# Performance work log

Hardware: AMD Instinct MI355X
Metric: run time of the kernel (lower is better)

The kernel has to match this reference:

```python
import math
import jax, jax.numpy as jnp
import numpy as np

B, N, D, H = 2, 2048, 1024, 16

def setup_inputs() -> dict:
    key = jax.random.key(0)
    ks = jax.random.split(key, 5)
    x = jax.random.normal(ks[0], (B, N, D), dtype=jnp.float32)
    # causal mask: True = masked (matches masked_fill semantics)
    mask = jnp.broadcast_to(jnp.triu(jnp.ones((N, N), dtype=bool), k=1), (B, N, N))
    sc = 0.02
    Wqkv = jax.random.normal(ks[1], (3 * D, D), dtype=jnp.float32) * sc
    bqkv = jax.random.normal(ks[2], (3 * D,), dtype=jnp.float32) * sc
    Wo = jax.random.normal(ks[3], (D, D), dtype=jnp.float32) * sc
    bo = jax.random.normal(ks[4], (D,), dtype=jnp.float32) * sc
    return {"x": x, "mask": mask, "Wqkv": Wqkv, "bqkv": bqkv, "Wo": Wo, "bo": bo}

def reference(x, mask, Wqkv, bqkv, Wo, bo):
    b, n, d = x.shape
    h = H
    s = d // h
    qkv = x @ Wqkv.T + bqkv                       # [b, n, 3d]
    q, k, v = jnp.split(qkv, 3, axis=2)           # each [b, n, d]
    def heads(z):
        return z.reshape(b, n, h, s).transpose(0, 2, 1, 3)  # [b, h, n, s]
    q, k, v = heads(q), heads(k), heads(v)
    q = q / jnp.asarray(math.sqrt(s), q.dtype)
    a = jnp.einsum('bhqs,bhks->bhqk', q, k)       # [b, h, n, n]
    a = jnp.where(mask[:, None, :, :], -jnp.inf, a)
    a = jax.nn.softmax(a, axis=-1)
    y = jnp.einsum('bhqk,bhks->bhqs', a, v)       # [b, h, n, s]
    y = y.transpose(0, 2, 1, 3).reshape(b, n, d)
    return y @ Wo.T + bo
```

## Files before the change

kernel.cpp:

```cpp
#include <hip/hip_runtime.h>
#include <hip/hip_bf16.h>
#include <stdint.h>

#define BB 2
#define NN 2048
#define DD 1024
#define HH 16
#define SS 64

typedef short short8 __attribute__((ext_vector_type(8)));
typedef float f32x4 __attribute__((ext_vector_type(4)));

__device__ __forceinline__ float bf2f(uint16_t u) {
    return __uint_as_float(((uint32_t)u) << 16);
}
__device__ __forceinline__ uint16_t f2bf(float f) {
    uint32_t u = __float_as_uint(f);
    return (uint16_t)((u + 0x7FFFu + ((u >> 16) & 1u)) >> 16);
}
__device__ __forceinline__ short8 cvt8(float4 a, float4 b) {
    short8 s;
    s[0] = (short)f2bf(a.x); s[1] = (short)f2bf(a.y);
    s[2] = (short)f2bf(a.z); s[3] = (short)f2bf(a.w);
    s[4] = (short)f2bf(b.x); s[5] = (short)f2bf(b.y);
    s[6] = (short)f2bf(b.z); s[7] = (short)f2bf(b.w);
    return s;
}

__device__ __forceinline__ void load_lds16(const uint16_t* g, uint16_t* l) {
    __builtin_amdgcn_global_load_lds(
        (const __attribute__((address_space(1))) void*)g,
        (__attribute__((address_space(3))) void*)l, 16, 0, 0);
}

#define XE  (4096 * 1024)
#define WQE (3072 * 1024)
#define WOE (1024 * 1024)

__global__ __launch_bounds__(256) void cvt_all(
    const float* __restrict__ x, const float* __restrict__ wq,
    const float* __restrict__ wo, uint16_t* __restrict__ dst)
{
    int i = (blockIdx.x * 256 + threadIdx.x) * 8;
    const float* src;
    int off;
    if (i < XE)            { src = x;  off = i; }
    else if (i < XE + WQE) { src = wq; off = i - XE; }
    else                   { src = wo; off = i - XE - WQE; }
    float4 a = *(const float4*)(src + off);
    float4 b = *(const float4*)(src + off + 4);
    *(short8*)(dst + i) = cvt8(a, b);
}

__global__ __launch_bounds__(256) void gemm_qkv(
    const uint16_t* __restrict__ X, const uint16_t* __restrict__ W,
    const float* __restrict__ bias,
    uint16_t* __restrict__ Qb, uint16_t* __restrict__ Kb, uint16_t* __restrict__ Vt)
{
    __shared__ __align__(16) uint16_t smem[18432];
    uint16_t* As0 = smem;
    uint16_t* As1 = smem + 4096;
    uint16_t* Bs0 = smem + 8192;
    uint16_t* Bs1 = smem + 12288;

    const int tid = threadIdx.x;
    const int w = tid >> 6, l = tid & 63;
    const int lq = l & 15, lg = l >> 4;
    const int wm = w >> 1, wn = w & 1;

    const int flat = blockIdx.x + blockIdx.y * 24;
    const int xcd = flat & 7, g = flat >> 3;
    const int n0 = (xcd * 3 + (g % 3)) * 128;
    const int m0 = (g / 3) * 128;

    f32x4 acc[4][4] = {};

    for (int k0 = 0; k0 < 1024; k0 += 64) {
        __syncthreads();
        #pragma unroll
        for (int j = 0; j < 2; ++j) {
            const int c = (j * 4 + w) * 64 + l;
            const size_t ra = (size_t)(m0 + (c >> 2)) * 1024 + k0 + (c & 3) * 8;
            const size_t rb = (size_t)(n0 + (c >> 2)) * 1024 + k0 + (c & 3) * 8;
            load_lds16(X + ra,      As0 + (j * 4 + w) * 512);
            load_lds16(X + ra + 32, As1 + (j * 4 + w) * 512);
            load_lds16(W + rb,      Bs0 + (j * 4 + w) * 512);
            load_lds16(W + rb + 32, Bs1 + (j * 4 + w) * 512);
        }
        __syncthreads();
        short8 af[4], bfr[4];
        #pragma unroll
        for (int mi = 0; mi < 4; ++mi)
            af[mi] = *(const short8*)&As0[(wm * 64 + mi * 16 + lq) * 32 + lg * 8];
        #pragma unroll
        for (int ni = 0; ni < 4; ++ni)
            bfr[ni] = *(const short8*)&Bs0[(wn * 64 + ni * 16 + lq) * 32 + lg * 8];
        #pragma unroll
        for (int mi = 0; mi < 4; ++mi)
            #pragma unroll
            for (int ni = 0; ni < 4; ++ni)
                acc[mi][ni] = __builtin_amdgcn_mfma_f32_16x16x32_bf16(
                    af[mi], bfr[ni], acc[mi][ni], 0, 0, 0);
        #pragma unroll
        for (int mi = 0; mi < 4; ++mi)
            af[mi] = *(const short8*)&As1[(wm * 64 + mi * 16 + lq) * 32 + lg * 8];
        #pragma unroll
        for (int ni = 0; ni < 4; ++ni)
            bfr[ni] = *(const short8*)&Bs1[(wn * 64 + ni * 16 + lq) * 32 + lg * 8];
        #pragma unroll
        for (int mi = 0; mi < 4; ++mi)
            #pragma unroll
            for (int ni = 0; ni < 4; ++ni)
                acc[mi][ni] = __builtin_amdgcn_mfma_f32_16x16x32_bf16(
                    af[mi], bfr[ni], acc[mi][ni], 0, 0, 0);
    }

    __syncthreads();
    const int part = n0 >> 10;
    const int hh = ((n0 + wn * 64) & 1023) >> 6;
    const int mrow0 = m0 + wm * 64;
    const int bh = (mrow0 >> 11) * 16 + hh;
    const int tok0 = mrow0 & 2047;
    const float scl = (part == 0) ? 0.125f * 1.44269504089f : 1.0f;

    float bias4[4];
    #pragma unroll
    for (int ni = 0; ni < 4; ++ni)
        bias4[ni] = bias[n0 + wn * 64 + ni * 16 + lq];

    uint16_t* T = smem + w * 4608;
    if (part < 2) {
        #pragma unroll
        for (int mi = 0; mi < 4; ++mi)
            #pragma unroll
            for (int ni = 0; ni < 4; ++ni)
                #pragma unroll
                for (int r = 0; r < 4; ++r)
                    T[(mi * 16 + lg * 4 + r) * 72 + ni * 16 + lq] =
                        f2bf((acc[mi][ni][r] + bias4[ni]) * scl);
    } else {
        #pragma unroll
        for (int mi = 0; mi < 4; ++mi)
            #pragma unroll
            for (int ni = 0; ni < 4; ++ni)
                #pragma unroll
                for (int r = 0; r < 4; ++r)
                    T[(ni * 16 + lq) * 72 + mi * 16 + lg * 4 + r] =
                        f2bf(acc[mi][ni][r] + bias4[ni]);
    }

    const int a0 = l >> 3, b8 = (l & 7) * 8;
    #pragma unroll
    for (int i = 0; i < 8; ++i) {
        int a = i * 8 + a0;
        short8 u = *(short8*)&T[a * 72 + b8];
        uint16_t* p;
        if (part < 2) {
            uint16_t* dst = (part == 0) ? Qb : Kb;
            p = dst + ((size_t)bh * 2048 + tok0 + a) * 64 + b8;
        } else {
            p = Vt + ((size_t)bh * 64 + a) * 2048 + tok0 + b8;
        }
        *(short8*)p = u;
    }
}

__device__ __forceinline__ void loadK8(const uint16_t* kp, short8 (&d)[8]) {
    #pragma unroll
    for (int n = 0; n < 4; ++n) {
        d[2 * n]     = *(const short8*)(kp + n * 1024);
        d[2 * n + 1] = *(const short8*)(kp + n * 1024 + 32);
    }
}
__device__ __forceinline__ void loadV8(const uint16_t* vp, short8 (&d)[8]) {
    #pragma unroll
    for (int n = 0; n < 4; ++n) {
        d[2 * n]     = *(const short8*)(vp + n * 32768);
        d[2 * n + 1] = *(const short8*)(vp + n * 32768 + 32);
    }
}

#define DEFER_THR 11.5f

__global__ __launch_bounds__(128) void attn_mfma(
    const uint16_t* __restrict__ Q, const uint16_t* __restrict__ K,
    const uint16_t* __restrict__ Vt, uint16_t* __restrict__ Y)
{
    const int id = blockIdx.x;
    const int bh = id & 31;
    const int xp = id >> 5;

    const int wv = threadIdx.x >> 6;
    const int lane = threadIdx.x & 63;
    const int lq = lane & 15;
    const int lg = lane >> 4;

    __shared__ __align__(16) uint16_t Pl[2][2][16][72];
    __shared__ float  My[32][68];
    __shared__ float2 Mml[32];

    const uint16_t* Kb = K + (size_t)bh * (2048 * 64);
    const uint16_t* Vb = Vt + (size_t)bh * (64 * 2048);
    const int b = bh >> 4, h = bh & 15;

    for (int half = 0; half < 2; ++half) {
        const int blk = half ? (63 - xp) : xp;
        const int qt = blk >> 1;
        const int q0 = blk * 32;

        short8 qf[2][2];
        #pragma unroll
        for (int sub = 0; sub < 2; ++sub) {
            const uint16_t* qb = Q + ((size_t)bh * 2048 + q0 + sub * 16 + lq) * 64 + lg * 8;
            qf[sub][0] = *(const short8*)qb;
            qf[sub][1] = *(const short8*)(qb + 32);
        }

        f32x4 y[2][4] = {};
        float m[2]    = {-INFINITY, -INFINITY};
        float lsum[2] = {0.f, 0.f};

        const uint16_t* kp = Kb + ((size_t)(wv * 64 + lq)) * 64 + lg * 8;
        const uint16_t* vp = Vb + (size_t)lq * 2048 + wv * 64 + lg * 8;

        short8 kf[8], vv[8];
        loadK8(kp, kf);

        auto step = [&](int kv0, const uint16_t* vcur, const uint16_t* knext,
                        bool domask, bool pref) {
            loadV8(vcur, vv);

            f32x4 z[2][4];
            __builtin_amdgcn_s_setprio(1);
            #pragma unroll
            for (int sub = 0; sub < 2; ++sub)
                #pragma unroll
                for (int n = 0; n < 4; ++n) {
                    f32x4 t = {};
                    t = __builtin_amdgcn_mfma_f32_16x16x32_bf16(kf[2 * n], qf[sub][0], t, 0, 0, 0);
                    z[sub][n] = __builtin_amdgcn_mfma_f32_16x16x32_bf16(kf[2 * n + 1], qf[sub][1], t, 0, 0, 0);
                }
            __builtin_amdgcn_s_setprio(0);

            if (pref) loadK8(knext, kf);

            if (domask) {
                #pragma unroll
                for (int sub = 0; sub < 2; ++sub) {
                    const int qrow = q0 + sub * 16 + lq;
                    #pragma unroll
                    for (int n = 0; n < 4; ++n) {
                        const int kvb = kv0 + n * 16 + lg * 4;
                        #pragma unroll
                        for (int r = 0; r < 4; ++r)
                            if (kvb + r > qrow) z[sub][n][r] = -INFINITY;
                    }
                }
            }

            float mt[2];
            #pragma unroll
            for (int sub = 0; sub < 2; ++sub) {
                float t = -INFINITY;
                #pragma unroll
                for (int n = 0; n < 4; ++n)
                    #pragma unroll
                    for (int r = 0; r < 4; ++r)
                        t = fmaxf(t, z[sub][n][r]);
                mt[sub] = t;
            }
            const float g = fmaxf(mt[0] - m[0], mt[1] - m[1]);
            const bool skip = __all(g <= DEFER_THR);

            if (!skip) {
                #pragma unroll
                for (int sub = 0; sub < 2; ++sub) {
                    float mf = fmaxf(mt[sub], __shfl_xor(mt[sub], 16));
                    mf = fmaxf(mf, __shfl_xor(mf, 32));
                    const float mn = fmaxf(m[sub], mf);
                    const float sc = exp2f(m[sub] - mn);
                    m[sub] = mn;
                    lsum[sub] *= sc;
                    float scy[4];
                    #pragma unroll
                    for (int r = 0; r < 4; ++r) scy[r] = __shfl(sc, lg * 4 + r);
                    #pragma unroll
                    for (int n = 0; n < 4; ++n)
                        #pragma unroll
                        for (int r = 0; r < 4; ++r)
                            y[sub][n][r] *= scy[r];
                }
            }

            float ps[2] = {0.f, 0.f};
            #pragma unroll
            for (int sub = 0; sub < 2; ++sub) {
                #pragma unroll
                for (int n = 0; n < 4; ++n) {
                    float e0 = exp2f(z[sub][n][0] - m[sub]);
                    float e1 = exp2f(z[sub][n][1] - m[sub]);
                    float e2 = exp2f(z[sub][n][2] - m[sub]);
                    float e3 = exp2f(z[sub][n][3] - m[sub]);
                    ps[sub] += (e0 + e1) + (e2 + e3);
                    uint32_t p0, p1;
                    asm("v_cvt_pk_bf16_f32 %0, %1, %2" : "=v"(p0) : "v"(e0), "v"(e1));
                    asm("v_cvt_pk_bf16_f32 %0, %1, %2" : "=v"(p1) : "v"(e2), "v"(e3));
                    uint2 u; u.x = p0; u.y = p1;
                    *(uint2*)&Pl[wv][sub][lq][n * 16 + lg * 4] = u;
                }
            }
            lsum[0] += ps[0];
            lsum[1] += ps[1];

            short8 pa[2][2];
            #pragma unroll
            for (int sub = 0; sub < 2; ++sub) {
                pa[sub][0] = *(short8*)&Pl[wv][sub][lq][lg * 8];
                pa[sub][1] = *(short8*)&Pl[wv][sub][lq][lg * 8 + 32];
            }

            __builtin_amdgcn_s_setprio(1);
            #pragma unroll
            for (int sub = 0; sub < 2; ++sub)
                #pragma unroll
                for (int n = 0; n < 4; ++n) {
                    y[sub][n] = __builtin_amdgcn_mfma_f32_16x16x32_bf16(pa[sub][0], vv[2 * n], y[sub][n], 0, 0, 0);
                    y[sub][n] = __builtin_amdgcn_mfma_f32_16x16x32_bf16(pa[sub][1], vv[2 * n + 1], y[sub][n], 0, 0, 0);
                }
            __builtin_amdgcn_s_setprio(0);
        };

        if (wv <= qt) {
            int kt = wv;
            for (; kt + 2 <= qt; kt += 2) {
                step(kt * 64, vp, kp + 8192, false, true);
                kp += 8192;
                vp += 128;
            }
            step(kt * 64, vp, kp, kt == qt, false);
        }

        float ls[2];
        #pragma unroll
        for (int sub = 0; sub < 2; ++sub) {
            float t = lsum[sub];
            t += __shfl_xor(t, 16);
            t += __shfl_xor(t, 32);
            ls[sub] = t;
        }

        if (wv == 1) {
            #pragma unroll
            for (int sub = 0; sub < 2; ++sub) {
                #pragma unroll
                for (int n = 0; n < 4; ++n)
                    #pragma unroll
                    for (int r = 0; r < 4; ++r)
                        My[sub * 16 + lg * 4 + r][n * 16 + lq] = y[sub][n][r];
                if (lg == 0) Mml[sub * 16 + lq] = make_float2(m[sub], ls[sub]);
            }
        }
        __syncthreads();
        if (wv == 0) {
            #pragma unroll
            for (int sub = 0; sub < 2; ++sub) {
                float2 o = Mml[sub * 16 + lq];
                const float m1 = o.x, l1 = o.y;
                const float mx = fmaxf(m[sub], m1);
                const float w0 = exp2f(m[sub] - mx);
                const float w1 = exp2f(m1 - mx);
                const float inv = 1.0f / (ls[sub] * w0 + l1 * w1);
                const float f0 = w0 * inv, f1 = w1 * inv;
                float f0r[4], f1r[4];
                #pragma unroll
                for (int r = 0; r < 4; ++r) {
                    f0r[r] = __shfl(f0, lg * 4 + r);
                    f1r[r] = __shfl(f1, lg * 4 + r);
                }
                #pragma unroll
                for (int r = 0; r < 4; ++r) {
                    int token = b * 2048 + q0 + sub * 16 + lg * 4 + r;
                    uint16_t* yrow = Y + (size_t)token * 1024 + h * 64;
                    #pragma unroll
                    for (int n = 0; n < 4; ++n) {
                        float val = y[sub][n][r] * f0r[r] +
                                    My[sub * 16 + lg * 4 + r][n * 16 + lq] * f1r[r];
                        yrow[n * 16 + lq] = f2bf(val);
                    }
                }
            }
        }
        __syncthreads();
    }
}

__global__ __launch_bounds__(256) void gemm_proj(
    const uint16_t* __restrict__ Yin, const uint16_t* __restrict__ W,
    const float* __restrict__ bias, float* __restrict__ out)
{
    __shared__ __align__(16) uint16_t smem[16384];
    uint16_t* As0 = smem;
    uint16_t* As1 = smem + 4096;
    uint16_t* Bs0 = smem + 8192;
    uint16_t* Bs1 = smem + 12288;

    const int tid = threadIdx.x;
    const int w = tid >> 6, l = tid & 63;
    const int lq = l & 15, lg = l >> 4;
    const int wm = w >> 1, wn = w & 1;

    const int flat = blockIdx.x + blockIdx.y * 8;
    const int n0 = (flat & 7) * 128;
    const int m0 = (flat >> 3) * 128;

    f32x4 acc[4][4] = {};

    for (int k0 = 0; k0 < 1024; k0 += 64) {
        __syncthreads();
        #pragma unroll
        for (int j = 0; j < 2; ++j) {
            const int c = (j * 4 + w) * 64 + l;
            const size_t ra = (size_t)(m0 + (c >> 2)) * 1024 + k0 + (c & 3) * 8;
            const size_t rb = (size_t)(n0 + (c >> 2)) * 1024 + k0 + (c & 3) * 8;
            load_lds16(Yin + ra,      As0 + (j * 4 + w) * 512);
            load_lds16(Yin + ra + 32, As1 + (j * 4 + w) * 512);
            load_lds16(W + rb,        Bs0 + (j * 4 + w) * 512);
            load_lds16(W + rb + 32,   Bs1 + (j * 4 + w) * 512);
        }
        __syncthreads();
        short8 af[4], bfr[4];
        #pragma unroll
        for (int mi = 0; mi < 4; ++mi)
            af[mi] = *(const short8*)&As0[(wm * 64 + mi * 16 + lq) * 32 + lg * 8];
        #pragma unroll
        for (int ni = 0; ni < 4; ++ni)
            bfr[ni] = *(const short8*)&Bs0[(wn * 64 + ni * 16 + lq) * 32 + lg * 8];
        #pragma unroll
        for (int mi = 0; mi < 4; ++mi)
            #pragma unroll
            for (int ni = 0; ni < 4; ++ni)
                acc[mi][ni] = __builtin_amdgcn_mfma_f32_16x16x32_bf16(
                    af[mi], bfr[ni], acc[mi][ni], 0, 0, 0);
        #pragma unroll
        for (int mi = 0; mi < 4; ++mi)
            af[mi] = *(const short8*)&As1[(wm * 64 + mi * 16 + lq) * 32 + lg * 8];
        #pragma unroll
        for (int ni = 0; ni < 4; ++ni)
            bfr[ni] = *(const short8*)&Bs1[(wn * 64 + ni * 16 + lq) * 32 + lg * 8];
        #pragma unroll
        for (int mi = 0; mi < 4; ++mi)
            #pragma unroll
            for (int ni = 0; ni < 4; ++ni)
                acc[mi][ni] = __builtin_amdgcn_mfma_f32_16x16x32_bf16(
                    af[mi], bfr[ni], acc[mi][ni], 0, 0, 0);
    }

    const int mrow0 = m0 + wm * 64;
    const int ncol0 = n0 + wn * 64;
    float bias4[4];
    #pragma unroll
    for (int ni = 0; ni < 4; ++ni)
        bias4[ni] = bias[ncol0 + ni * 16 + lq];

    #pragma unroll
    for (int mi = 0; mi < 4; ++mi)
        #pragma unroll
        for (int r = 0; r < 4; ++r) {
            const size_t rowoff = (size_t)(mrow0 + mi * 16 + lg * 4 + r) * 1024;
            #pragma unroll
            for (int ni = 0; ni < 4; ++ni)
                out[rowoff + ncol0 + ni * 16 + lq] = acc[mi][ni][r] + bias4[ni];
        }
}


extern "C" void kernel_launch(void* const* d_in, const int* in_sizes, int n_in,
                              void* d_out, int out_size, void* d_ws, size_t ws_size,
                              hipStream_t stream) {
    const float* x    = (const float*)d_in[0];
    const float* Wqkv = (const float*)d_in[2];
    const float* bqkv = (const float*)d_in[3];
    const float* Wo   = (const float*)d_in[4];
    const float* bo   = (const float*)d_in[5];

    const size_t QK = (size_t)BB * HH * NN * SS;

    uint16_t* Xb  = (uint16_t*)d_ws;
    uint16_t* Wqb = Xb + XE;
    uint16_t* Wob = Wqb + WQE;
    uint16_t* Qb  = Wob + WOE;
    uint16_t* Kb  = Qb + QK;
    uint16_t* Vt  = Kb + QK;
    uint16_t* Yb  = Vt + QK;

    cvt_all<<<(XE + WQE + WOE) / 8 / 256, 256, 0, stream>>>(x, Wqkv, Wo, Xb);
    gemm_qkv<<<dim3(24, 32), 256, 0, stream>>>(Xb, Wqb, bqkv, Qb, Kb, Vt);
    attn_mfma<<<1024, 128, 0, stream>>>(Qb, Kb, Vt, Yb);
    gemm_proj<<<dim3(8, 32), 256, 0, stream>>>(Yb, Wob, bo, (float*)d_out);
}
```

Before: 140.7 us.

## Process 64-query tiles per block, reusing each K/V load across four sub-tiles

Each attention block now handles a single 64-row query tile instead of two 32-row tiles from opposite ends of the causal triangle. Every K and V fragment load from global memory now feeds four 16-row sub-tiles instead of two, halving K/V traffic per query row. Blocks are launched longest-first (descending tile index) in place of the paired balancing. The cost is more registers for the Q fragments, accumulators and softmax state, which may lower occupancy, and the per-block work is less balanced than the paired scheme.

```diff
diff --git a/kernel.cpp b/kernel.cpp
--- a/kernel.cpp
+++ b/kernel.cpp
@@ -188,7 +188,9 @@
 {
     const int id = blockIdx.x;
     const int bh = id & 31;
-    const int xp = id >> 5;
+    const int blk = 31 - (id >> 5);
+    const int qt = blk;
+    const int q0 = blk * 64;
 
     const int wv = threadIdx.x >> 6;
     const int lane = threadIdx.x & 63;
@@ -196,201 +198,198 @@
     const int lg = lane >> 4;
 
     __shared__ __align__(16) uint16_t Pl[2][2][16][72];
-    __shared__ float  My[32][68];
-    __shared__ float2 Mml[32];
+    __shared__ float  My[64][68];
+    __shared__ float2 Mml[64];
 
     const uint16_t* Kb = K + (size_t)bh * (2048 * 64);
     const uint16_t* Vb = Vt + (size_t)bh * (64 * 2048);
     const int b = bh >> 4, h = bh & 15;
 
-    for (int half = 0; half < 2; ++half) {
-        const int blk = half ? (63 - xp) : xp;
-        const int qt = blk >> 1;
-        const int q0 = blk * 32;
-
-        short8 qf[2][2];
-        #pragma unroll
-        for (int sub = 0; sub < 2; ++sub) {
-            const uint16_t* qb = Q + ((size_t)bh * 2048 + q0 + sub * 16 + lq) * 64 + lg * 8;
-            qf[sub][0] = *(const short8*)qb;
-            qf[sub][1] = *(const short8*)(qb + 32);
-        }
-
-        f32x4 y[2][4] = {};
-        float m[2]    = {-INFINITY, -INFINITY};
-        float lsum[2] = {0.f, 0.f};
-
-        const uint16_t* kp = Kb + ((size_t)(wv * 64 + lq)) * 64 + lg * 8;
-        const uint16_t* vp = Vb + (size_t)lq * 2048 + wv * 64 + lg * 8;
-
-        short8 kf[8], vv[8];
-        loadK8(kp, kf);
-
-        auto step = [&](int kv0, const uint16_t* vcur, const uint16_t* knext,
-                        bool domask, bool pref) {
-            loadV8(vcur, vv);
-
-            f32x4 z[2][4];
-            __builtin_amdgcn_s_setprio(1);
-            #pragma unroll
-            for (int sub = 0; sub < 2; ++sub)
+    short8 qf[4][2];
+    #pragma unroll
+    for (int sub = 0; sub < 4; ++sub) {
+        const uint16_t* qb = Q + ((size_t)bh * 2048 + q0 + sub * 16 + lq) * 64 + lg * 8;
+        qf[sub][0] = *(const short8*)qb;
+        qf[sub][1] = *(const short8*)(qb + 32);
+    }
+
+    f32x4 y[4][4] = {};
+    float m[4]    = {-INFINITY, -INFINITY, -INFINITY, -INFINITY};
+    float lsum[4] = {0.f, 0.f, 0.f, 0.f};
+
+    const uint16_t* kp = Kb + ((size_t)(wv * 64 + lq)) * 64 + lg * 8;
+    const uint16_t* vp = Vb + (size_t)lq * 2048 + wv * 64 + lg * 8;
+
+    short8 kf[8], vv[8];
+
+    auto qkpair = [&](f32x4 (&z)[2][4], int s0) {
+        __builtin_amdgcn_s_setprio(1);
+        #pragma unroll
+        for (int p = 0; p < 2; ++p)
+            #pragma unroll
+            for (int n = 0; n < 4; ++n) {
+                f32x4 t = {};
+                t = __builtin_amdgcn_mfma_f32_16x16x32_bf16(kf[2 * n], qf[s0 + p][0], t, 0, 0, 0);
+                z[p][n] = __builtin_amdgcn_mfma_f32_16x16x32_bf16(kf[2 * n + 1], qf[s0 + p][1], t, 0, 0, 0);
+            }
+        __builtin_amdgcn_s_setprio(0);
+    };
+
+    auto smpv = [&](f32x4 (&z)[2][4], int s0, int kv0, bool domask) {
+        if (domask) {
+            #pragma unroll
+            for (int p = 0; p < 2; ++p) {
+                const int qrow = q0 + (s0 + p) * 16 + lq;
                 #pragma unroll
                 for (int n = 0; n < 4; ++n) {
-                    f32x4 t = {};
-                    t = __builtin_amdgcn_mfma_f32_16x16x32_bf16(kf[2 * n], qf[sub][0], t, 0, 0, 0);
-                    z[sub][n] = __builtin_amdgcn_mfma_f32_16x16x32_bf16(kf[2 * n + 1], qf[sub][1], t, 0, 0, 0);
+                    const int kvb = kv0 + n * 16 + lg * 4;
+                    #pragma unroll
+                    for (int r = 0; r < 4; ++r)
+                        if (kvb + r > qrow) z[p][n][r] = -INFINITY;
                 }
-            __builtin_amdgcn_s_setprio(0);
-
-            if (pref) loadK8(knext, kf);
-
-            if (domask) {
-                #pragma unroll
-                for (int sub = 0; sub < 2; ++sub) {
-                    const int qrow = q0 + sub * 16 + lq;
-                    #pragma unroll
-                    for (int n = 0; n < 4; ++n) {
-                        const int kvb = kv0 + n * 16 + lg * 4;
-                        #pragma unroll
-                        for (int r = 0; r < 4; ++r)
-                            if (kvb + r > qrow) z[sub][n][r] = -INFINITY;
-                    }
-                }
-            }
-
-            float mt[2];
-            #pragma unroll
-            for (int sub = 0; sub < 2; ++sub) {
-                float t = -INFINITY;
+            }
+        }
+        float mt[2];
+        #pragma unroll
+        for (int p = 0; p < 2; ++p) {
+            float t = -INFINITY;
+            #pragma unroll
+            for (int n = 0; n < 4; ++n)
+                #pragma unroll
+                for (int r = 0; r < 4; ++r)
+                    t = fmaxf(t, z[p][n][r]);
+            mt[p] = t;
+        }
+        const float g = fmaxf(mt[0] - m[s0], mt[1] - m[s0 + 1]);
+        const bool skip = __all(g <= DEFER_THR);
+        if (!skip) {
+            #pragma unroll
+            for (int p = 0; p < 2; ++p) {
+                const int s = s0 + p;
+                float mf = fmaxf(mt[p], __shfl_xor(mt[p], 16));
+                mf = fmaxf(mf, __shfl_xor(mf, 32));
+                const float mn = fmaxf(m[s], mf);
+                const float sc = exp2f(m[s] - mn);
+                m[s] = mn;
+                lsum[s] *= sc;
+                float scy[4];
+                #pragma unroll
+                for (int r = 0; r < 4; ++r) scy[r] = __shfl(sc, lg * 4 + r);
                 #pragma unroll
                 for (int n = 0; n < 4; ++n)
                     #pragma unroll
                     for (int r = 0; r < 4; ++r)
-                        t = fmaxf(t, z[sub][n][r]);
-                mt[sub] = t;
-            }
-            const float g = fmaxf(mt[0] - m[0], mt[1] - m[1]);
-            const bool skip = __all(g <= DEFER_THR);
-
-            if (!skip) {
-                #pragma unroll
-                for (int sub = 0; sub < 2; ++sub) {
-                    float mf = fmaxf(mt[sub], __shfl_xor(mt[sub], 16));
-                    mf = fmaxf(mf, __shfl_xor(mf, 32));
-                    const float mn = fmaxf(m[sub], mf);
-                    const float sc = exp2f(m[sub] - mn);
-                    m[sub] = mn;
-                    lsum[sub] *= sc;
-                    float scy[4];
-                    #pragma unroll
-                    for (int r = 0; r < 4; ++r) scy[r] = __shfl(sc, lg * 4 + r);
-                    #pragma unroll
-                    for (int n = 0; n < 4; ++n)
-                        #pragma unroll
-                        for (int r = 0; r < 4; ++r)
-                            y[sub][n][r] *= scy[r];
+                        y[s][n][r] *= scy[r];
+            }
+        }
+        float ps[2] = {0.f, 0.f};
+        #pragma unroll
+        for (int p = 0; p < 2; ++p) {
+            const int s = s0 + p;
+            #pragma unroll
+            for (int n = 0; n < 4; ++n) {
+                float e0 = exp2f(z[p][n][0] - m[s]);
+                float e1 = exp2f(z[p][n][1] - m[s]);
+                float e2 = exp2f(z[p][n][2] - m[s]);
+                float e3 = exp2f(z[p][n][3] - m[s]);
+                ps[p] += (e0 + e1) + (e2 + e3);
+                uint32_t p0, p1;
+                asm("v_cvt_pk_bf16_f32 %0, %1, %2" : "=v"(p0) : "v"(e0), "v"(e1));
+                asm("v_cvt_pk_bf16_f32 %0, %1, %2" : "=v"(p1) : "v"(e2), "v"(e3));
+                uint2 u; u.x = p0; u.y = p1;
+                *(uint2*)&Pl[wv][p][lq][n * 16 + lg * 4] = u;
+            }
+        }
+        lsum[s0] += ps[0];
+        lsum[s0 + 1] += ps[1];
+
+        short8 pa[2][2];
+        #pragma unroll
+        for (int p = 0; p < 2; ++p) {
+            pa[p][0] = *(short8*)&Pl[wv][p][lq][lg * 8];
+            pa[p][1] = *(short8*)&Pl[wv][p][lq][lg * 8 + 32];
+        }
+        __builtin_amdgcn_s_setprio(1);
+        #pragma unroll
+        for (int p = 0; p < 2; ++p) {
+            const int s = s0 + p;
+            #pragma unroll
+            for (int n = 0; n < 4; ++n) {
+                y[s][n] = __builtin_amdgcn_mfma_f32_16x16x32_bf16(pa[p][0], vv[2 * n], y[s][n], 0, 0, 0);
+                y[s][n] = __builtin_amdgcn_mfma_f32_16x16x32_bf16(pa[p][1], vv[2 * n + 1], y[s][n], 0, 0, 0);
+            }
+        }
+        __builtin_amdgcn_s_setprio(0);
+    };
+
+    if (wv <= qt) {
+        loadK8(kp, kf);
+        int kt = wv;
+        while (true) {
+            const bool last = (kt + 2 > qt);
+            const bool domask = (kt == qt);
+            const int kv0 = kt * 64;
+            loadV8(vp, vv);
+            f32x4 z[2][4];
+            qkpair(z, 0);
+            smpv(z, 0, kv0, domask);
+            qkpair(z, 2);
+            if (!last) loadK8(kp + 8192, kf);
+            smpv(z, 2, kv0, domask);
+            if (last) break;
+            kp += 8192; vp += 128; kt += 2;
+        }
+    }
+
+    float ls[4];
+    #pragma unroll
+    for (int s = 0; s < 4; ++s) {
+        float t = lsum[s];
+        t += __shfl_xor(t, 16);
+        t += __shfl_xor(t, 32);
+        ls[s] = t;
+    }
+
+    if (wv == 1) {
+        #pragma unroll
+        for (int s = 0; s < 4; ++s) {
+            #pragma unroll
+            for (int n = 0; n < 4; ++n)
+                #pragma unroll
+                for (int r = 0; r < 4; ++r)
+                    My[s * 16 + lg * 4 + r][n * 16 + lq] = y[s][n][r];
+            if (lg == 0) Mml[s * 16 + lq] = make_float2(m[s], ls[s]);
+        }
+    }
+    __syncthreads();
+    if (wv == 0) {
+        #pragma unroll
+        for (int s = 0; s < 4; ++s) {
+            float2 o = Mml[s * 16 + lq];
+            const float m1 = o.x, l1 = o.y;
+            const float mx = fmaxf(m[s], m1);
+            const float w0 = exp2f(m[s] - mx);
+            const float w1 = exp2f(m1 - mx);
+            const float inv = 1.0f / (ls[s] * w0 + l1 * w1);
+            const float f0 = w0 * inv, f1 = w1 * inv;
+            float f0r[4], f1r[4];
+            #pragma unroll
+            for (int r = 0; r < 4; ++r) {
+                f0r[r] = __shfl(f0, lg * 4 + r);
+                f1r[r] = __shfl(f1, lg * 4 + r);
+            }
+            #pragma unroll
+            for (int r = 0; r < 4; ++r) {
+                int token = b * 2048 + q0 + s * 16 + lg * 4 + r;
+                uint16_t* yrow = Y + (size_t)token * 1024 + h * 64;
+                #pragma unroll
+                for (int n = 0; n < 4; ++n) {
+                    float val = y[s][n][r] * f0r[r] +
+                                My[s * 16 + lg * 4 + r][n * 16 + lq] * f1r[r];
+                    yrow[n * 16 + lq] = f2bf(val);
                 }
             }
-
-            float ps[2] = {0.f, 0.f};
-            #pragma unroll
-            for (int sub = 0; sub < 2; ++sub) {
-                #pragma unroll
-                for (int n = 0; n < 4; ++n) {
-                    float e0 = exp2f(z[sub][n][0] - m[sub]);
-                    float e1 = exp2f(z[sub][n][1] - m[sub]);
-                    float e2 = exp2f(z[sub][n][2] - m[sub]);
-                    float e3 = exp2f(z[sub][n][3] - m[sub]);
-                    ps[sub] += (e0 + e1) + (e2 + e3);
-                    uint32_t p0, p1;
-                    asm("v_cvt_pk_bf16_f32 %0, %1, %2" : "=v"(p0) : "v"(e0), "v"(e1));
-                    asm("v_cvt_pk_bf16_f32 %0, %1, %2" : "=v"(p1) : "v"(e2), "v"(e3));
-                    uint2 u; u.x = p0; u.y = p1;
-                    *(uint2*)&Pl[wv][sub][lq][n * 16 + lg * 4] = u;
-                }
-            }
-            lsum[0] += ps[0];
-            lsum[1] += ps[1];
-
-            short8 pa[2][2];
-            #pragma unroll
-            for (int sub = 0; sub < 2; ++sub) {
-                pa[sub][0] = *(short8*)&Pl[wv][sub][lq][lg * 8];
-                pa[sub][1] = *(short8*)&Pl[wv][sub][lq][lg * 8 + 32];
-            }
-
-            __builtin_amdgcn_s_setprio(1);
-            #pragma unroll
-            for (int sub = 0; sub < 2; ++sub)
-                #pragma unroll
-                for (int n = 0; n < 4; ++n) {
-                    y[sub][n] = __builtin_amdgcn_mfma_f32_16x16x32_bf16(pa[sub][0], vv[2 * n], y[sub][n], 0, 0, 0);
-                    y[sub][n] = __builtin_amdgcn_mfma_f32_16x16x32_bf16(pa[sub][1], vv[2 * n + 1], y[sub][n], 0, 0, 0);
-                }
-            __builtin_amdgcn_s_setprio(0);
-        };
-
-        if (wv <= qt) {
-            int kt = wv;
-            for (; kt + 2 <= qt; kt += 2) {
-                step(kt * 64, vp, kp + 8192, false, true);
-                kp += 8192;
-                vp += 128;
-            }
-            step(kt * 64, vp, kp, kt == qt, false);
-        }
-
-        float ls[2];
-        #pragma unroll
-        for (int sub = 0; sub < 2; ++sub) {
-            float t = lsum[sub];
-            t += __shfl_xor(t, 16);
-            t += __shfl_xor(t, 32);
-            ls[sub] = t;
-        }
-
-        if (wv == 1) {
-            #pragma unroll
-            for (int sub = 0; sub < 2; ++sub) {
-                #pragma unroll
-                for (int n = 0; n < 4; ++n)
-                    #pragma unroll
-                    for (int r = 0; r < 4; ++r)
-                        My[sub * 16 + lg * 4 + r][n * 16 + lq] = y[sub][n][r];
-                if (lg == 0) Mml[sub * 16 + lq] = make_float2(m[sub], ls[sub]);
-            }
-        }
-        __syncthreads();
-        if (wv == 0) {
-            #pragma unroll
-            for (int sub = 0; sub < 2; ++sub) {
-                float2 o = Mml[sub * 16 + lq];
-                const float m1 = o.x, l1 = o.y;
-                const float mx = fmaxf(m[sub], m1);
-                const float w0 = exp2f(m[sub] - mx);
-                const float w1 = exp2f(m1 - mx);
-                const float inv = 1.0f / (ls[sub] * w0 + l1 * w1);
-                const float f0 = w0 * inv, f1 = w1 * inv;
-                float f0r[4], f1r[4];
-                #pragma unroll
-                for (int r = 0; r < 4; ++r) {
-                    f0r[r] = __shfl(f0, lg * 4 + r);
-                    f1r[r] = __shfl(f1, lg * 4 + r);
-                }
-                #pragma unroll
-                for (int r = 0; r < 4; ++r) {
-                    int token = b * 2048 + q0 + sub * 16 + lg * 4 + r;
-                    uint16_t* yrow = Y + (size_t)token * 1024 + h * 64;
-                    #pragma unroll
-                    for (int n = 0; n < 4; ++n) {
-                        float val = y[sub][n][r] * f0r[r] +
-                                    My[sub * 16 + lg * 4 + r][n * 16 + lq] * f1r[r];
-                        yrow[n * 16 + lq] = f2bf(val);
-                    }
-                }
-            }
-        }
-        __syncthreads();
+        }
     }
 }
 
```

Result: faster. 123.9 us (median of 3 runs) (-11.9%).
